# Performance work log

Hardware: AMD Instinct MI355X
Metric: run time of the kernel (lower is better)

## Reference

```python
import jax, jax.numpy as jnp
import numpy as np

SCALES = (4, 2, 2)  # config.latent_structure.scaling_factors


def expand_length(x, scale):
    # Faithful to conv_transpose1d with an all-ones (D, D, scale) kernel at
    # stride=scale: out[b, l*scale + j, d] = sum_d' x[b, l, d'] for all j, d.
    # i.e. channel-sum broadcast to all channels, repeated `scale` times in L.
    s = jnp.sum(x, axis=-1, keepdims=True)            # [B, L, 1]
    y = jnp.broadcast_to(s, x.shape)                  # [B, L, D]
    return jnp.repeat(y, scale, axis=1)               # [B, L*scale, D]


def setup_inputs() -> dict:
    key = jax.random.key(0)
    k0, k1, k2, k3 = jax.random.split(key, 4)
    B, L, D0 = 8, 64, 256
    D1, D2, D3 = 512, 768, 768
    scale = 0.02
    return {
        "z_1": jax.random.normal(k0, (B, L, D0), jnp.float32),
        "W1": jax.random.normal(k1, (D0, D1), jnp.float32) * scale,
        "b1": jnp.zeros((D1,), jnp.float32),
        "W2": jax.random.normal(k2, (D1, D2), jnp.float32) * scale,
        "b2": jnp.zeros((D2,), jnp.float32),
        "W3": jax.random.normal(k3, (D2, D3), jnp.float32) * scale,
        "b3": jnp.zeros((D3,), jnp.float32),
    }


def reference(z_1, W1, b1, W2, b2, W3, b3):
    x = z_1
    for s in SCALES:                 # scaled_inputs is None -> plain loop
        x = expand_length(x, s)
    x = jnp.einsum("bld,de->ble", x, W1) + b1   # embedding_upscale1
    x = expand_length(x, SCALES[1])
    x = jnp.einsum("bld,de->ble", x, W2) + b2   # embedding_upscale2
    x = expand_length(x, SCALES[2])
    x = jnp.einsum("bld,de->ble", x, W3) + b3   # embedding_upscale3
    return x  # [8, 4096, 768]
```

## Files before the change

kernel.cpp:

```cpp
#include <hip/hip_runtime.h>

typedef float f4 __attribute__((ext_vector_type(4)));

#define NF_W1P  0
#define NF_W2P  32
#define NF_B1   128
#define NF_B2   129
#define NF_S0   130
#define NF_CW3P 656

__device__ __forceinline__ float wave_reduce(float v) {
#pragma unroll
    for (int off = 32; off; off >>= 1) v += __shfl_down(v, off, 64);
    return v;
}

__device__ __forceinline__ float block_reduce_256(float v) {
    __shared__ float sm[4];
    v = wave_reduce(v);
    int lane = threadIdx.x & 63, wid = threadIdx.x >> 6;
    if (lane == 0) sm[wid] = v;
    __syncthreads();
    if (threadIdx.x == 0) v = sm[0] + sm[1] + sm[2] + sm[3];
    return v;
}

__global__ __launch_bounds__(256) void k_reduce(
    const float* __restrict__ z1, const float* __restrict__ W1,
    const float* __restrict__ b1, const float* __restrict__ W2,
    const float* __restrict__ b2, const float* __restrict__ W3,
    float* __restrict__ f) {
    const int blk = blockIdx.x, tid = threadIdx.x;
    if (blk < 128) {
        const float* p = (blk < 32) ? (W1 + blk * 4096) : (W2 + (blk - 32) * 4096);
        float s = 0.f;
#pragma unroll
        for (int i = 0; i < 16; ++i) s += p[tid + i * 256];
        s = block_reduce_256(s);
        if (tid == 0) f[blk] = s;
    } else if (blk == 128) {
        float s = b1[tid] + b1[tid + 256];
        s = block_reduce_256(s);
        if (tid == 0) f[NF_B1] = s;
    } else if (blk == 129) {
        float s = b2[tid] + b2[tid + 256] + b2[tid + 512];
        s = block_reduce_256(s);
        if (tid == 0) f[NF_B2] = s;
    } else if (blk < 258) {
        const int lane = tid & 63, wid = tid >> 6;
        const int row = (blk - 130) * 4 + wid;
        const float* p = z1 + row * 256;
        float s = p[lane] + p[lane + 64] + p[lane + 128] + p[lane + 192];
        s = wave_reduce(s);
        if (lane == 0) f[NF_S0 + row] = s;
    } else {
        const int g = blk - 258;
        const int cg = g % 3, rg = g / 3;
        const int e = cg * 256 + tid;
        const float* p = W3 + rg * 96 * 768 + e;
        float s = 0.f;
#pragma unroll 8
        for (int d = 0; d < 96; ++d) s += p[d * 768];
        f[NF_CW3P + rg * 768 + e] = s;
    }
}

__global__ __launch_bounds__(256) void k_write(
    const float* __restrict__ f, const float* __restrict__ b3,
    float* __restrict__ out) {
    __shared__ float cw_sm[768];
    __shared__ float b_sm[768];
    __shared__ float u_sm;
    const int tid = threadIdx.x;

#pragma unroll
    for (int k = 0; k < 3; ++k) {
        const int e = tid + k * 256;
        float c = 0.f;
#pragma unroll
        for (int r = 0; r < 8; ++r) c += f[NF_CW3P + r * 768 + e];
        cw_sm[e] = c;
        b_sm[e] = b3[e];
    }
    if (tid < 64) {
        float a = (tid < 32) ? f[NF_W1P + tid] : 0.f;
        float b = f[NF_W2P + tid] + ((tid < 32) ? f[NF_W2P + 64 + tid] : 0.f);
#pragma unroll
        for (int off = 32; off; off >>= 1) {
            a += __shfl_down(a, off, 64);
            b += __shfl_down(b, off, 64);
        }
        if (tid == 0) {
            const int uidx = blockIdx.x >> 2;
            u_sm = (65536.0f * f[NF_S0 + uidx] * a + f[NF_B1]) * b + f[NF_B2];
        }
    }
    __syncthreads();

    const float u = u_sm;
    const int lane = tid & 63, wid = tid >> 6;
    const f4* __restrict__ cw4 = (const f4*)cw_sm;
    const f4* __restrict__ b4  = (const f4*)b_sm;
#pragma unroll
    for (int r = 0; r < 4; ++r) {
        const int row = blockIdx.x * 16 + wid * 4 + r;
        f4* o = (f4*)(out + (size_t)row * 768);
#pragma unroll
        for (int k = 0; k < 3; ++k) {
            const int e4 = lane + k * 64;
            const f4 c = cw4[e4];
            const f4 b = b4[e4];
            f4 v;
            v.x = fmaf(u, c.x, b.x);
            v.y = fmaf(u, c.y, b.y);
            v.z = fmaf(u, c.z, b.z);
            v.w = fmaf(u, c.w, b.w);
            __builtin_nontemporal_store(v, &o[e4]);
        }
    }
}

extern "C" void kernel_launch(void* const* d_in, const int* in_sizes, int n_in,
                              void* d_out, int out_size, void* d_ws, size_t ws_size,
                              hipStream_t stream) {
    const float* z1 = (const float*)d_in[0];
    const float* W1 = (const float*)d_in[1];
    const float* b1 = (const float*)d_in[2];
    const float* W2 = (const float*)d_in[3];
    const float* b2 = (const float*)d_in[4];
    const float* W3 = (const float*)d_in[5];
    const float* b3 = (const float*)d_in[6];
    float* out = (float*)d_out;
    float* f = (float*)d_ws;

    k_reduce<<<282, 256, 0, stream>>>(z1, W1, b1, W2, b2, W3, f);
    k_write<<<2048, 256, 0, stream>>>(f, b3, out);
}
```

Baseline: 28.51 us.

## Finalize reductions in last-arriving reduce block; simplify write kernel prologue

Adds an atomic counter so the last block of the reduce kernel combines the partial W3 column sums into a final vector and precomputes per-row scalars u for all 512 rows. The write kernel then skips its per-block 8-way partial sum, shared-memory staging, wave reductions and barrier, and reads the precomputed vectors directly from global memory into registers. This trades redundant per-block prologue work across 2048 blocks for an extra memset launch and a serialized tail in one reduce block.

```diff
diff --git a/kernel.cpp b/kernel.cpp
--- a/kernel.cpp
+++ b/kernel.cpp
@@ -8,6 +8,9 @@
 #define NF_B2   129
 #define NF_S0   130
 #define NF_CW3P 656
+#define NF_CW3  6800
+#define NF_U    7568
+#define NI_CNT  8080
 
 __device__ __forceinline__ float wave_reduce(float v) {
 #pragma unroll
@@ -63,15 +66,18 @@
         for (int d = 0; d < 96; ++d) s += p[d * 768];
         f[NF_CW3P + rg * 768 + e] = s;
     }
-}
 
-__global__ __launch_bounds__(256) void k_write(
-    const float* __restrict__ f, const float* __restrict__ b3,
-    float* __restrict__ out) {
-    __shared__ float cw_sm[768];
-    __shared__ float b_sm[768];
-    __shared__ float u_sm;
-    const int tid = threadIdx.x;
+    __shared__ int last_sm;
+    __shared__ float s12_sm[2];
+    __syncthreads();
+    if (tid == 0) {
+        __threadfence();
+        int old = atomicAdd((int*)(f + NI_CNT), 1);
+        last_sm = (old == 281);
+    }
+    __syncthreads();
+    if (!last_sm) return;
+    __threadfence();
 
 #pragma unroll
     for (int k = 0; k < 3; ++k) {
@@ -79,8 +85,7 @@
         float c = 0.f;
 #pragma unroll
         for (int r = 0; r < 8; ++r) c += f[NF_CW3P + r * 768 + e];
-        cw_sm[e] = c;
-        b_sm[e] = b3[e];
+        f[NF_CW3 + e] = c;
     }
     if (tid < 64) {
         float a = (tid < 32) ? f[NF_W1P + tid] : 0.f;
@@ -90,33 +95,44 @@
             a += __shfl_down(a, off, 64);
             b += __shfl_down(b, off, 64);
         }
-        if (tid == 0) {
-            const int uidx = blockIdx.x >> 2;
-            u_sm = (65536.0f * f[NF_S0 + uidx] * a + f[NF_B1]) * b + f[NF_B2];
-        }
+        if (tid == 0) { s12_sm[0] = a; s12_sm[1] = b; }
     }
     __syncthreads();
+    const float S1 = s12_sm[0], S2 = s12_sm[1];
+    const float B1 = f[NF_B1], B2 = f[NF_B2];
+#pragma unroll
+    for (int k = 0; k < 2; ++k) {
+        const int t = tid + k * 256;
+        f[NF_U + t] = (65536.0f * f[NF_S0 + t] * S1 + B1) * S2 + B2;
+    }
+}
 
-    const float u = u_sm;
+__global__ __launch_bounds__(256) void k_write(
+    const float* __restrict__ f, const float* __restrict__ b3,
+    float* __restrict__ out) {
+    const int tid = threadIdx.x;
     const int lane = tid & 63, wid = tid >> 6;
-    const f4* __restrict__ cw4 = (const f4*)cw_sm;
-    const f4* __restrict__ b4  = (const f4*)b_sm;
+    const float u = f[NF_U + (blockIdx.x >> 2)];
+    const f4* __restrict__ cw4 = (const f4*)(f + NF_CW3);
+    const f4* __restrict__ b4  = (const f4*)b3;
+    f4 v[3];
+#pragma unroll
+    for (int k = 0; k < 3; ++k) {
+        const int e4 = lane + k * 64;
+        const f4 c = cw4[e4];
+        const f4 b = b4[e4];
+        v[k].x = fmaf(u, c.x, b.x);
+        v[k].y = fmaf(u, c.y, b.y);
+        v[k].z = fmaf(u, c.z, b.z);
+        v[k].w = fmaf(u, c.w, b.w);
+    }
 #pragma unroll
     for (int r = 0; r < 4; ++r) {
         const int row = blockIdx.x * 16 + wid * 4 + r;
         f4* o = (f4*)(out + (size_t)row * 768);
 #pragma unroll
-        for (int k = 0; k < 3; ++k) {
-            const int e4 = lane + k * 64;
-            const f4 c = cw4[e4];
-            const f4 b = b4[e4];
-            f4 v;
-            v.x = fmaf(u, c.x, b.x);
-            v.y = fmaf(u, c.y, b.y);
-            v.z = fmaf(u, c.z, b.z);
-            v.w = fmaf(u, c.w, b.w);
-            __builtin_nontemporal_store(v, &o[e4]);
-        }
+        for (int k = 0; k < 3; ++k)
+            __builtin_nontemporal_store(v[k], &o[lane + k * 64]);
     }
 }
 
@@ -133,6 +149,7 @@
     float* out = (float*)d_out;
     float* f = (float*)d_ws;
 
+    hipMemsetAsync((char*)d_ws + NI_CNT * sizeof(float), 0, 4, stream);
     k_reduce<<<282, 256, 0, stream>>>(z1, W1, b1, W2, b2, W3, f);
     k_write<<<2048, 256, 0, stream>>>(f, b3, out);
 }
```

New measurement: 38.26 us. 34.2% more time.
